# Kernel tuning notes

Measured on AMD Instinct MI355X. Metric: run time of the kernel, lower is better.

## Reference

```python
import jax, jax.numpy as jnp
import numpy as np

EPS = 1e-6

def _feature_map(x):
    # elu(x) + 1  (positive feature map)
    return jax.nn.elu(x) + 1.0

def setup_inputs() -> dict:
    key = jax.random.key(0)
    kq, kk, kv = jax.random.split(key, 3)
    N, L, S, H, D = 8, 4096, 4096, 8, 64
    return {
        "queries": jax.random.normal(kq, (N, L, H, D), dtype=jnp.float32),
        "keys": jax.random.normal(kk, (N, S, H, D), dtype=jnp.float32),
        "values": jax.random.normal(kv, (N, S, H, D), dtype=jnp.float32),
        "q_mask": jnp.ones((N, L), dtype=jnp.float32),
        "kv_mask": jnp.ones((N, S), dtype=jnp.float32),
    }

def reference(queries, keys, values, q_mask, kv_mask):
    Q = _feature_map(queries)                      # [N,L,H,D]
    K = _feature_map(keys)                         # [N,S,H,D]
    Q = Q * q_mask[:, :, None, None]
    kvm = kv_mask[:, :, None, None]
    K = K * kvm
    V = values * kvm
    S_len = V.shape[1]
    scale = 1.0 / S_len
    Vs = V * scale
    KV = jnp.einsum('nshd,nshv->nhdv', K, Vs)      # [N,H,D,D]
    # normalizer: Q . sum_s K   (intended math of the source einsum)
    Z = 1.0 / (jnp.einsum('nlhd,nhd->nlh', Q, K.sum(axis=1)) + EPS)
    out = jnp.einsum('nlhd,nhdv,nlh->nlhv', Q, KV, Z) * S_len
    return out
```

## Files before the change

kernel.cpp:

```cpp
#include <hip/hip_runtime.h>
#include <hip/hip_bf16.h>

#define NB 8
#define LQ 4096
#define SK 4096
#define NH 8
#define DD 64
#define NPAIR (NB*NH)
#define KVSZ (DD*DD + DD)
#define FRAGW 768

typedef short v8s __attribute__((ext_vector_type(8)));
typedef float v4f __attribute__((ext_vector_type(4)));
union U8 { v8s s; unsigned int u[4]; uint4 q; };

__device__ __forceinline__ float fmap(float x) {
    return x > 0.f ? x + 1.f : __expf(x);
}
__device__ __forceinline__ unsigned short bf_hi(float x) {
    unsigned int u = __float_as_uint(x);
    return (unsigned short)((u + 0x7FFFu + ((u >> 16) & 1u)) >> 16);
}
__device__ __forceinline__ float bf_f(unsigned short b) {
    return __uint_as_float(((unsigned int)b) << 16);
}
__device__ __forceinline__ uint2 packsplit2(float x0, float x1) {
    union { __hip_bfloat162 b; unsigned int u; } h, l;
    h.b = __float22bfloat162_rn(make_float2(x0, x1));
    float r0 = x0 - __uint_as_float(h.u << 16);
    float r1 = x1 - __uint_as_float(h.u & 0xFFFF0000u);
    l.b = __float22bfloat162_rn(make_float2(r0, r1));
    uint2 r; r.x = h.u; r.y = l.u;
    return r;
}
#define MFMA(A, B, C) __builtin_amdgcn_mfma_f32_16x16x32_bf16((A), (B), (C), 0, 0, 0)

__device__ __forceinline__ void gload16(const float* g, float* lds) {
    __builtin_amdgcn_global_load_lds(
        (const __attribute__((address_space(1))) unsigned int*)g,
        (__attribute__((address_space(3))) unsigned int*)lds, 16, 0, 0);
}

__global__ __launch_bounds__(256, 3) void kv_partial_kernel(
    const float* __restrict__ K, const float* __restrict__ V,
    const float* __restrict__ kvm, float* __restrict__ partial, int CH)
{
    int bx = blockIdx.x;
    int chunk = bx % CH;
    int pair  = bx / CH;
    int nb = pair >> 3, h = pair & 7;
    int tid = threadIdx.x, w = tid >> 6, lane = tid & 63;
    int g = lane >> 4, c16 = lane & 15;

    __shared__ float Kl[2][2048];
    __shared__ float Vl[2][2048];

    v4f acc[4];
    v4f z4 = {0.f, 0.f, 0.f, 0.f};
#pragma unroll
    for (int nn = 0; nn < 4; ++nn) acc[nn] = z4;
    float ksum = 0.f;

    int SC = SK / CH;
    int tiles = SC >> 5;
    int rowbase = nb * SK + chunk * SC;

    int srow0 = (lane >> 4);
    int dp    = (lane & 15) << 2;

    auto STAGE = [&](int b, int t) {
#pragma unroll
        for (int i = 0; i < 2; ++i) {
            int I = 2 * w + i;
            int s = I * 4 + srow0;
            int dl = dp ^ (((s >> 3) & 1) << 4);
            size_t gb = (size_t)(rowbase + (t << 5) + s) * (NH * DD) + h * DD + dl;
            gload16(K + gb, &Kl[b][I * 256]);
            gload16(V + gb, &Vl[b][I * 256]);
        }
    };

    auto COMPUTE = [&](int b, const float* mr) {
        float xa[8];
#pragma unroll
        for (int j = 0; j < 8; ++j) {
            int s = 8 * g + j;
            float kv_ = Kl[b][s * 64 + ((16 * w + c16) ^ (((s >> 3) & 1) << 4))];
            xa[j] = fmap(kv_) * mr[j];
            ksum += xa[j];
        }
        U8 ah, al;
#pragma unroll
        for (int p = 0; p < 4; ++p) {
            uint2 pw = packsplit2(xa[2 * p], xa[2 * p + 1]);
            ah.u[p] = pw.x; al.u[p] = pw.y;
        }
#pragma unroll
        for (int nn = 0; nn < 4; ++nn) {
            float xb[8];
#pragma unroll
            for (int j = 0; j < 8; ++j) {
                int s = 8 * g + j;
                xb[j] = Vl[b][s * 64 + ((16 * nn + c16) ^ (((s >> 3) & 1) << 4))] * mr[j];
            }
            U8 bh, bl;
#pragma unroll
            for (int p = 0; p < 4; ++p) {
                uint2 pw = packsplit2(xb[2 * p], xb[2 * p + 1]);
                bh.u[p] = pw.x; bl.u[p] = pw.y;
            }
            acc[nn] = MFMA(ah.s, bh.s, acc[nn]);
            acc[nn] = MFMA(al.s, bh.s, acc[nn]);
            acc[nn] = MFMA(ah.s, bl.s, acc[nn]);
        }
    };

    float mr0[8], mr1[8];
    auto MLOADR = [&](float* mr, int t) {
#pragma unroll
        for (int j = 0; j < 8; ++j)
            mr[j] = kvm[rowbase + (t << 5) + 8 * g + j];
    };

    STAGE(0, 0); MLOADR(mr0, 0);
    __syncthreads();
    for (int t = 0; t < tiles; t += 2) {
        if (t + 1 < tiles) { STAGE(1, t + 1); MLOADR(mr1, t + 1); }
        COMPUTE(0, mr0);
        __syncthreads();
        if (t + 1 < tiles) {
            if (t + 2 < tiles) { STAGE(0, t + 2); MLOADR(mr0, t + 2); }
            COMPUTE(1, mr1);
            __syncthreads();
        }
    }

    ksum += __shfl_xor(ksum, 16);
    ksum += __shfl_xor(ksum, 32);
    float* dst = partial + ((size_t)chunk * NPAIR + pair) * KVSZ;
    if (lane < 16) dst[4096 + 16 * w + c16] = ksum;
#pragma unroll
    for (int nn = 0; nn < 4; ++nn)
#pragma unroll
        for (int jj = 0; jj < 4; ++jj)
            dst[(16 * w + 4 * g + jj) * 64 + 16 * nn + c16] = acc[nn][jj];
}

__global__ __launch_bounds__(256) void kv_reduce_kernel(
    const float* __restrict__ partial, float* __restrict__ kvf, int CH)
{
    int i = blockIdx.x * 256 + threadIdx.x;
    if (i >= NPAIR * KVSZ) return;
    float s = 0.f;
    for (int c = 0; c < CH; ++c) s += partial[(size_t)c * NPAIR * KVSZ + i];
    kvf[i] = s;
}

__global__ __launch_bounds__(256) void kv_pack_kernel(
    const float* __restrict__ kvf, uint4* __restrict__ frag)
{
    int pair = blockIdx.x;
    int t = threadIdx.x;
    __shared__ float kvr[KVSZ];
    const float* src = kvf + (size_t)pair * KVSZ;
    for (int e = t; e < KVSZ / 4; e += 256)
        *(float4*)&kvr[4 * e] = *(const float4*)(src + 4 * e);
    __syncthreads();

    for (int e = t; e < FRAGW; e += 256) {
        int i4 = e >> 6, lane = e & 63;
        int g = lane >> 4, c16 = lane & 15;
        unsigned int wd[4];
        if (i4 < 8) {
            int ks = i4 >> 2, nn = i4 & 3;
#pragma unroll
            for (int p = 0; p < 4; ++p) {
                float x0 = kvr[(32 * ks + 8 * g + 2 * p) * 64 + 16 * nn + c16];
                float x1 = kvr[(32 * ks + 8 * g + 2 * p + 1) * 64 + 16 * nn + c16];
                wd[p] = (unsigned int)bf_hi(x0) | ((unsigned int)bf_hi(x1) << 16);
            }
        } else {
            int j = i4 - 8, ks = j & 1, lo = j >> 1;
#pragma unroll
            for (int p = 0; p < 4; ++p) {
                unsigned int wp = 0;
                if (c16 == 0) {
                    float x0 = kvr[4096 + 32 * ks + 8 * g + 2 * p];
                    float x1 = kvr[4096 + 32 * ks + 8 * g + 2 * p + 1];
                    unsigned short h0 = bf_hi(x0), h1 = bf_hi(x1);
                    if (lo)
                        wp = (unsigned int)bf_hi(x0 - bf_f(h0)) |
                             ((unsigned int)bf_hi(x1 - bf_f(h1)) << 16);
                    else
                        wp = (unsigned int)h0 | ((unsigned int)h1 << 16);
                }
                wd[p] = wp;
            }
        }
        uint4 o; o.x = wd[0]; o.y = wd[1]; o.z = wd[2]; o.w = wd[3];
        frag[(size_t)pair * FRAGW + e] = o;
    }
}

__global__ __launch_bounds__(256) void attn_out_kernel(
    const float* __restrict__ Q, const float* __restrict__ qm,
    const uint4* __restrict__ frag, float* __restrict__ out)
{
    int bx = blockIdx.x;
    int pair = bx >> 5;
    int rb   = bx & 31;
    int nb = pair >> 3, h = pair & 7;
    int lane = threadIdx.x & 63;
    int w    = threadIdx.x >> 6;
    int g    = lane >> 4;
    int c16  = lane & 15;

    const uint4* fb = frag + (size_t)pair * FRAGW;
    U8 Bh[2][4], Bkh[2], Bkl[2];
#pragma unroll
    for (int ks = 0; ks < 2; ++ks)
#pragma unroll
        for (int nn = 0; nn < 4; ++nn)
            Bh[ks][nn].q = fb[(ks * 4 + nn) * 64 + lane];
    Bkh[0].q = fb[8 * 64 + lane];
    Bkh[1].q = fb[9 * 64 + lane];
    Bkl[0].q = fb[10 * 64 + lane];
    Bkl[1].q = fb[11 * 64 + lane];

    float4 qA[2][4];
    float qmA[2];

    auto QLOAD = [&](int it, float4* qr, float& qmv) {
        int row = rb * 128 + (w + 4 * it) * 16 + c16;
        qmv = qm[nb * LQ + row];
        const float* qrow = Q + ((size_t)((nb * LQ + row) * NH + h)) * DD;
        qr[0] = *(const float4*)(qrow + 8 * g);
        qr[1] = *(const float4*)(qrow + 8 * g + 4);
        qr[2] = *(const float4*)(qrow + 8 * g + 32);
        qr[3] = *(const float4*)(qrow + 8 * g + 36);
    };

    v4f z4 = {0.f, 0.f, 0.f, 0.f};
    QLOAD(0, qA[0], qmA[0]);
#pragma unroll
    for (int it = 0; it < 2; ++it) {
        if (it == 0) QLOAD(1, qA[1], qmA[1]);
        const float4* qr = qA[it];
        float qmv = qmA[it];

        U8 Ah[2], Al[2];
#pragma unroll
        for (int ks = 0; ks < 2; ++ks) {
            float qv[8] = {qr[2*ks].x, qr[2*ks].y, qr[2*ks].z, qr[2*ks].w,
                           qr[2*ks+1].x, qr[2*ks+1].y, qr[2*ks+1].z, qr[2*ks+1].w};
#pragma unroll
            for (int p = 0; p < 4; ++p) {
                uint2 pw = packsplit2(fmap(qv[2*p]) * qmv, fmap(qv[2*p+1]) * qmv);
                Ah[ks].u[p] = pw.x;
                Al[ks].u[p] = pw.y;
            }
        }

        v4f a0 = z4, a1 = z4, a2 = z4, a3 = z4, a4 = z4;
#pragma unroll
        for (int ks = 0; ks < 2; ++ks) {
            a0 = MFMA(Ah[ks].s, Bh[ks][0].s, a0);
            a1 = MFMA(Ah[ks].s, Bh[ks][1].s, a1);
            a2 = MFMA(Ah[ks].s, Bh[ks][2].s, a2);
            a3 = MFMA(Ah[ks].s, Bh[ks][3].s, a3);
            a0 = MFMA(Al[ks].s, Bh[ks][0].s, a0);
            a1 = MFMA(Al[ks].s, Bh[ks][1].s, a1);
            a2 = MFMA(Al[ks].s, Bh[ks][2].s, a2);
            a3 = MFMA(Al[ks].s, Bh[ks][3].s, a3);
            a4 = MFMA(Ah[ks].s, Bkh[ks].s, a4);
            a4 = MFMA(Al[ks].s, Bkh[ks].s, a4);
            a4 = MFMA(Ah[ks].s, Bkl[ks].s, a4);
        }

        int row0 = rb * 128 + (w + 4 * it) * 16;
        int src = lane & 48;
#pragma unroll
        for (int jj = 0; jj < 4; ++jj) {
            float den = __shfl(a4[jj], src);
            float z = 1.f / (den + 1e-6f);
            size_t ob = ((size_t)((nb * LQ + row0 + 4 * g + jj) * NH + h)) * DD + c16;
            out[ob]      = a0[jj] * z;
            out[ob + 16] = a1[jj] * z;
            out[ob + 32] = a2[jj] * z;
            out[ob + 48] = a3[jj] * z;
        }
    }
}

extern "C" void kernel_launch(void* const* d_in, const int* in_sizes, int n_in,
                              void* d_out, int out_size, void* d_ws, size_t ws_size,
                              hipStream_t stream) {
    const float* Q   = (const float*)d_in[0];
    const float* K   = (const float*)d_in[1];
    const float* V   = (const float*)d_in[2];
    const float* qm  = (const float*)d_in[3];
    const float* kvm = (const float*)d_in[4];
    float* out = (float*)d_out;

    int CH = 16;
    while (CH > 1 && (size_t)(CH + 1) * NPAIR * KVSZ * sizeof(float) > ws_size) CH >>= 1;

    float* partial = (float*)d_ws;
    float* kvf = partial + (size_t)CH * NPAIR * KVSZ;
    uint4* frag = (uint4*)d_ws;

    kv_partial_kernel<<<dim3(NPAIR * CH), dim3(256), 0, stream>>>(K, V, kvm, partial, CH);
    kv_reduce_kernel<<<dim3((NPAIR * KVSZ + 255) / 256), dim3(256), 0, stream>>>(partial, kvf, CH);
    kv_pack_kernel<<<dim3(NPAIR), dim3(256), 0, stream>>>(kvf, frag);
    attn_out_kernel<<<dim3(NPAIR * 32), dim3(256), 0, stream>>>(Q, qm, frag, out);
}
```

Measured before the change: 81.93 us.

## Restructure KV partial kernel to load full rows across all heads per block

The KV-partial kernel now gives each 512-thread block one batch and sequence chunk across all 8 heads, one wave per head. It stages contiguous 2KB K/V rows (all heads) into LDS instead of strided 256B per-head slices. Each wave computes a full 64x64 KV tile with 16-row tiles, so half the lanes feed zeros into the MFMAs because the K=32 instruction is only half used. Chunk count doubles to 32, which doubles the partial-sum traffic through the reduce kernel, and register use per thread rises with 16 accumulators.

After: 93.35 us. +13.9%, slower.

```diff
diff --git a/kernel.cpp b/kernel.cpp
--- a/kernel.cpp
+++ b/kernel.cpp
@@ -9,6 +9,7 @@
 #define NPAIR (NB*NH)
 #define KVSZ (DD*DD + DD)
 #define FRAGW 768
+#define TS 16
 
 typedef short v8s __attribute__((ext_vector_type(8)));
 typedef float v4f __attribute__((ext_vector_type(4)));
@@ -41,109 +42,131 @@
         (__attribute__((address_space(3))) unsigned int*)lds, 16, 0, 0);
 }
 
-__global__ __launch_bounds__(256, 3) void kv_partial_kernel(
+__global__ __launch_bounds__(512, 2) void kv_partial_kernel(
     const float* __restrict__ K, const float* __restrict__ V,
     const float* __restrict__ kvm, float* __restrict__ partial, int CH)
 {
     int bx = blockIdx.x;
     int chunk = bx % CH;
-    int pair  = bx / CH;
-    int nb = pair >> 3, h = pair & 7;
+    int nb    = bx / CH;
     int tid = threadIdx.x, w = tid >> 6, lane = tid & 63;
     int g = lane >> 4, c16 = lane & 15;
 
-    __shared__ float Kl[2][2048];
-    __shared__ float Vl[2][2048];
-
-    v4f acc[4];
+    __shared__ float Kt[2][TS][512];
+    __shared__ float Vt[2][TS][512];
+
+    v4f acc[4][4];
     v4f z4 = {0.f, 0.f, 0.f, 0.f};
 #pragma unroll
-    for (int nn = 0; nn < 4; ++nn) acc[nn] = z4;
-    float ksum = 0.f;
+    for (int md = 0; md < 4; ++md)
+#pragma unroll
+        for (int nn = 0; nn < 4; ++nn) acc[md][nn] = z4;
+    float ksum[4] = {0.f, 0.f, 0.f, 0.f};
 
     int SC = SK / CH;
-    int tiles = SC >> 5;
+    int tiles = SC / TS;
     int rowbase = nb * SK + chunk * SC;
 
-    int srow0 = (lane >> 4);
-    int dp    = (lane & 15) << 2;
-
     auto STAGE = [&](int b, int t) {
 #pragma unroll
-        for (int i = 0; i < 2; ++i) {
-            int I = 2 * w + i;
-            int s = I * 4 + srow0;
-            int dl = dp ^ (((s >> 3) & 1) << 4);
-            size_t gb = (size_t)(rowbase + (t << 5) + s) * (NH * DD) + h * DD + dl;
-            gload16(K + gb, &Kl[b][I * 256]);
-            gload16(V + gb, &Vl[b][I * 256]);
+        for (int u = 0; u < 8; ++u) {
+            int unit = w * 8 + u;
+            int arr  = unit >> 5;
+            int row  = (unit >> 1) & 15;
+            int half = unit & 1;
+            size_t gb = ((size_t)(rowbase + t * TS + row)) * 512 + half * 256 + lane * 4;
+            if (arr == 0) gload16(K + gb, &Kt[b][row][half * 256]);
+            else          gload16(V + gb, &Vt[b][row][half * 256]);
         }
     };
 
+    auto MLOAD = [&](float* mr, int t) {
+        if (g < 2) {
+#pragma unroll
+            for (int j = 0; j < 8; ++j)
+                mr[j] = kvm[rowbase + t * TS + 8 * g + j];
+        }
+    };
+
     auto COMPUTE = [&](int b, const float* mr) {
-        float xa[8];
-#pragma unroll
-        for (int j = 0; j < 8; ++j) {
-            int s = 8 * g + j;
-            float kv_ = Kl[b][s * 64 + ((16 * w + c16) ^ (((s >> 3) & 1) << 4))];
-            xa[j] = fmap(kv_) * mr[j];
-            ksum += xa[j];
-        }
-        U8 ah, al;
-#pragma unroll
-        for (int p = 0; p < 4; ++p) {
-            uint2 pw = packsplit2(xa[2 * p], xa[2 * p + 1]);
-            ah.u[p] = pw.x; al.u[p] = pw.y;
-        }
+        U8 bh[4], bl[4];
 #pragma unroll
         for (int nn = 0; nn < 4; ++nn) {
-            float xb[8];
-#pragma unroll
-            for (int j = 0; j < 8; ++j) {
-                int s = 8 * g + j;
-                xb[j] = Vl[b][s * 64 + ((16 * nn + c16) ^ (((s >> 3) & 1) << 4))] * mr[j];
-            }
-            U8 bh, bl;
-#pragma unroll
-            for (int p = 0; p < 4; ++p) {
-                uint2 pw = packsplit2(xb[2 * p], xb[2 * p + 1]);
-                bh.u[p] = pw.x; bl.u[p] = pw.y;
-            }
-            acc[nn] = MFMA(ah.s, bh.s, acc[nn]);
-            acc[nn] = MFMA(al.s, bh.s, acc[nn]);
-            acc[nn] = MFMA(ah.s, bl.s, acc[nn]);
+            if (g < 2) {
+                float xb[8];
+#pragma unroll
+                for (int j = 0; j < 8; ++j)
+                    xb[j] = Vt[b][8 * g + j][w * 64 + 16 * nn + c16] * mr[j];
+#pragma unroll
+                for (int p = 0; p < 4; ++p) {
+                    uint2 pw = packsplit2(xb[2 * p], xb[2 * p + 1]);
+                    bh[nn].u[p] = pw.x; bl[nn].u[p] = pw.y;
+                }
+            } else {
+#pragma unroll
+                for (int p = 0; p < 4; ++p) { bh[nn].u[p] = 0u; bl[nn].u[p] = 0u; }
+            }
+        }
+#pragma unroll
+        for (int md = 0; md < 4; ++md) {
+            U8 ah, al;
+            if (g < 2) {
+                float xa[8];
+#pragma unroll
+                for (int j = 0; j < 8; ++j) {
+                    float x = fmap(Kt[b][8 * g + j][w * 64 + 16 * md + c16]) * mr[j];
+                    xa[j] = x;
+                    ksum[md] += x;
+                }
+#pragma unroll
+                for (int p = 0; p < 4; ++p) {
+                    uint2 pw = packsplit2(xa[2 * p], xa[2 * p + 1]);
+                    ah.u[p] = pw.x; al.u[p] = pw.y;
+                }
+            } else {
+#pragma unroll
+                for (int p = 0; p < 4; ++p) { ah.u[p] = 0u; al.u[p] = 0u; }
+            }
+#pragma unroll
+            for (int nn = 0; nn < 4; ++nn) {
+                acc[md][nn] = MFMA(ah.s, bh[nn].s, acc[md][nn]);
+                acc[md][nn] = MFMA(al.s, bh[nn].s, acc[md][nn]);
+                acc[md][nn] = MFMA(ah.s, bl[nn].s, acc[md][nn]);
+            }
         }
     };
 
-    float mr0[8], mr1[8];
-    auto MLOADR = [&](float* mr, int t) {
-#pragma unroll
-        for (int j = 0; j < 8; ++j)
-            mr[j] = kvm[rowbase + (t << 5) + 8 * g + j];
-    };
-
-    STAGE(0, 0); MLOADR(mr0, 0);
+    float mrA[8], mrB[8];
+    STAGE(0, 0); MLOAD(mrA, 0);
     __syncthreads();
     for (int t = 0; t < tiles; t += 2) {
-        if (t + 1 < tiles) { STAGE(1, t + 1); MLOADR(mr1, t + 1); }
-        COMPUTE(0, mr0);
+        if (t + 1 < tiles) { STAGE(1, t + 1); MLOAD(mrB, t + 1); }
+        COMPUTE(0, mrA);
         __syncthreads();
         if (t + 1 < tiles) {
-            if (t + 2 < tiles) { STAGE(0, t + 2); MLOADR(mr0, t + 2); }
-            COMPUTE(1, mr1);
+            if (t + 2 < tiles) { STAGE(0, t + 2); MLOAD(mrA, t + 2); }
+            COMPUTE(1, mrB);
             __syncthreads();
         }
     }
 
-    ksum += __shfl_xor(ksum, 16);
-    ksum += __shfl_xor(ksum, 32);
+#pragma unroll
+    for (int md = 0; md < 4; ++md) {
+        ksum[md] += __shfl_xor(ksum[md], 16);
+        ksum[md] += __shfl_xor(ksum[md], 32);
+    }
+    int pair = nb * 8 + w;
     float* dst = partial + ((size_t)chunk * NPAIR + pair) * KVSZ;
-    if (lane < 16) dst[4096 + 16 * w + c16] = ksum;
-#pragma unroll
-    for (int nn = 0; nn < 4; ++nn)
-#pragma unroll
-        for (int jj = 0; jj < 4; ++jj)
-            dst[(16 * w + 4 * g + jj) * 64 + 16 * nn + c16] = acc[nn][jj];
+    if (lane < 16)
+#pragma unroll
+        for (int md = 0; md < 4; ++md) dst[4096 + 16 * md + c16] = ksum[md];
+#pragma unroll
+    for (int md = 0; md < 4; ++md)
+#pragma unroll
+        for (int nn = 0; nn < 4; ++nn)
+#pragma unroll
+            for (int jj = 0; jj < 4; ++jj)
+                dst[(16 * md + 4 * g + jj) * 64 + 16 * nn + c16] = acc[md][nn][jj];
 }
 
 __global__ __launch_bounds__(256) void kv_reduce_kernel(
@@ -302,14 +325,14 @@
     const float* kvm = (const float*)d_in[4];
     float* out = (float*)d_out;
 
-    int CH = 16;
+    int CH = 32;
     while (CH > 1 && (size_t)(CH + 1) * NPAIR * KVSZ * sizeof(float) > ws_size) CH >>= 1;
 
     float* partial = (float*)d_ws;
     float* kvf = partial + (size_t)CH * NPAIR * KVSZ;
     uint4* frag = (uint4*)d_ws;
 
-    kv_partial_kernel<<<dim3(NPAIR * CH), dim3(256), 0, stream>>>(K, V, kvm, partial, CH);
+    kv_partial_kernel<<<dim3(NB * CH), dim3(512), 0, stream>>>(K, V, kvm, partial, CH);
     kv_reduce_kernel<<<dim3((NPAIR * KVSZ + 255) / 256), dim3(256), 0, stream>>>(partial, kvf, CH);
     kv_pack_kernel<<<dim3(NPAIR), dim3(256), 0, stream>>>(kvf, frag);
     attn_out_kernel<<<dim3(NPAIR * 32), dim3(256), 0, stream>>>(Q, qm, frag, out);
```

## Load K/V directly to registers with 2x2 MFMA tiles per wave

Applied to the files above, without the earlier changes.

Rewrites the KV partial kernel to drop the double-buffered LDS staging and barriers, with each thread loading its K and V elements straight from global memory into registers. Each wave now computes a 2x2 block of 16x16 tiles, a 32-row slice of the D dimension by a 32-column slice of V, instead of a 16x64 strip, so each wave converts fewer V fragments per step. The chunk count rises to 32 and the occupancy hint to 4 blocks per CU to expose more parallelism. The cost is strided, less coalesced 4-byte global loads with no prefetch overlap, and a larger partial buffer for the reduce kernel to read.

Measured after the change: 88.29 us. 1.08x slower.

```diff
diff --git a/kernel.cpp b/kernel.cpp
--- a/kernel.cpp
+++ b/kernel.cpp
@@ -35,13 +35,7 @@
 }
 #define MFMA(A, B, C) __builtin_amdgcn_mfma_f32_16x16x32_bf16((A), (B), (C), 0, 0, 0)
 
-__device__ __forceinline__ void gload16(const float* g, float* lds) {
-    __builtin_amdgcn_global_load_lds(
-        (const __attribute__((address_space(1))) unsigned int*)g,
-        (__attribute__((address_space(3))) unsigned int*)lds, 16, 0, 0);
-}
-
-__global__ __launch_bounds__(256, 3) void kv_partial_kernel(
+__global__ __launch_bounds__(256, 4) void kv_partial_kernel(
     const float* __restrict__ K, const float* __restrict__ V,
     const float* __restrict__ kvm, float* __restrict__ partial, int CH)
 {
@@ -51,99 +45,88 @@
     int nb = pair >> 3, h = pair & 7;
     int tid = threadIdx.x, w = tid >> 6, lane = tid & 63;
     int g = lane >> 4, c16 = lane & 15;
-
-    __shared__ float Kl[2][2048];
-    __shared__ float Vl[2][2048];
-
-    v4f acc[4];
+    int dh = w >> 1, vh = w & 1;
+
+    v4f acc[2][2];
     v4f z4 = {0.f, 0.f, 0.f, 0.f};
-#pragma unroll
-    for (int nn = 0; nn < 4; ++nn) acc[nn] = z4;
-    float ksum = 0.f;
+    acc[0][0] = z4; acc[0][1] = z4; acc[1][0] = z4; acc[1][1] = z4;
+    float ksum[2] = {0.f, 0.f};
 
     int SC = SK / CH;
     int tiles = SC >> 5;
     int rowbase = nb * SK + chunk * SC;
 
-    int srow0 = (lane >> 4);
-    int dp    = (lane & 15) << 2;
-
-    auto STAGE = [&](int b, int t) {
-#pragma unroll
-        for (int i = 0; i < 2; ++i) {
-            int I = 2 * w + i;
-            int s = I * 4 + srow0;
-            int dl = dp ^ (((s >> 3) & 1) << 4);
-            size_t gb = (size_t)(rowbase + (t << 5) + s) * (NH * DD) + h * DD + dl;
-            gload16(K + gb, &Kl[b][I * 256]);
-            gload16(V + gb, &Vl[b][I * 256]);
-        }
-    };
-
-    auto COMPUTE = [&](int b, const float* mr) {
-        float xa[8];
+    const float* Kp = K + (size_t)rowbase * (NH * DD) + h * DD + 32 * dh + c16;
+    const float* Vp = V + (size_t)rowbase * (NH * DD) + h * DD + 32 * vh + c16;
+    const float* Mp = kvm + rowbase + 8 * g;
+
+    for (int t = 0; t < tiles; ++t) {
+        float kb[16], vb[16], mb[8];
+        int s0 = (t << 5) + 8 * g;
 #pragma unroll
         for (int j = 0; j < 8; ++j) {
-            int s = 8 * g + j;
-            float kv_ = Kl[b][s * 64 + ((16 * w + c16) ^ (((s >> 3) & 1) << 4))];
-            xa[j] = fmap(kv_) * mr[j];
-            ksum += xa[j];
-        }
-        U8 ah, al;
-#pragma unroll
-        for (int p = 0; p < 4; ++p) {
-            uint2 pw = packsplit2(xa[2 * p], xa[2 * p + 1]);
-            ah.u[p] = pw.x; al.u[p] = pw.y;
-        }
-#pragma unroll
-        for (int nn = 0; nn < 4; ++nn) {
+            size_t off = (size_t)(s0 + j) * (NH * DD);
+            mb[j]     = Mp[(t << 5) + j];
+            kb[j]     = Kp[off];
+            kb[8 + j] = Kp[off + 16];
+            vb[j]     = Vp[off];
+            vb[8 + j] = Vp[off + 16];
+        }
+        U8 ah[2], al[2], bh[2], bl[2];
+#pragma unroll
+        for (int m = 0; m < 2; ++m) {
+            float xa[8];
+#pragma unroll
+            for (int j = 0; j < 8; ++j) xa[j] = fmap(kb[m * 8 + j]) * mb[j];
+            if (vh == 0) {
+#pragma unroll
+                for (int j = 0; j < 8; ++j) ksum[m] += xa[j];
+            }
+#pragma unroll
+            for (int p = 0; p < 4; ++p) {
+                uint2 pw = packsplit2(xa[2 * p], xa[2 * p + 1]);
+                ah[m].u[p] = pw.x; al[m].u[p] = pw.y;
+            }
+        }
+#pragma unroll
+        for (int n = 0; n < 2; ++n) {
             float xb[8];
 #pragma unroll
-            for (int j = 0; j < 8; ++j) {
-                int s = 8 * g + j;
-                xb[j] = Vl[b][s * 64 + ((16 * nn + c16) ^ (((s >> 3) & 1) << 4))] * mr[j];
-            }
-            U8 bh, bl;
+            for (int j = 0; j < 8; ++j) xb[j] = vb[n * 8 + j] * mb[j];
 #pragma unroll
             for (int p = 0; p < 4; ++p) {
                 uint2 pw = packsplit2(xb[2 * p], xb[2 * p + 1]);
-                bh.u[p] = pw.x; bl.u[p] = pw.y;
-            }
-            acc[nn] = MFMA(ah.s, bh.s, acc[nn]);
-            acc[nn] = MFMA(al.s, bh.s, acc[nn]);
-            acc[nn] = MFMA(ah.s, bl.s, acc[nn]);
-        }
-    };
-
-    float mr0[8], mr1[8];
-    auto MLOADR = [&](float* mr, int t) {
-#pragma unroll
-        for (int j = 0; j < 8; ++j)
-            mr[j] = kvm[rowbase + (t << 5) + 8 * g + j];
-    };
-
-    STAGE(0, 0); MLOADR(mr0, 0);
-    __syncthreads();
-    for (int t = 0; t < tiles; t += 2) {
-        if (t + 1 < tiles) { STAGE(1, t + 1); MLOADR(mr1, t + 1); }
-        COMPUTE(0, mr0);
-        __syncthreads();
-        if (t + 1 < tiles) {
-            if (t + 2 < tiles) { STAGE(0, t + 2); MLOADR(mr0, t + 2); }
-            COMPUTE(1, mr1);
-            __syncthreads();
-        }
-    }
-
-    ksum += __shfl_xor(ksum, 16);
-    ksum += __shfl_xor(ksum, 32);
+                bh[n].u[p] = pw.x; bl[n].u[p] = pw.y;
+            }
+        }
+#pragma unroll
+        for (int m = 0; m < 2; ++m)
+#pragma unroll
+            for (int n = 0; n < 2; ++n) {
+                acc[m][n] = MFMA(ah[m].s, bh[n].s, acc[m][n]);
+                acc[m][n] = MFMA(al[m].s, bh[n].s, acc[m][n]);
+                acc[m][n] = MFMA(ah[m].s, bl[n].s, acc[m][n]);
+            }
+    }
+
+#pragma unroll
+    for (int m = 0; m < 2; ++m) {
+        ksum[m] += __shfl_xor(ksum[m], 16);
+        ksum[m] += __shfl_xor(ksum[m], 32);
+    }
     float* dst = partial + ((size_t)chunk * NPAIR + pair) * KVSZ;
-    if (lane < 16) dst[4096 + 16 * w + c16] = ksum;
-#pragma unroll
-    for (int nn = 0; nn < 4; ++nn)
-#pragma unroll
-        for (int jj = 0; jj < 4; ++jj)
-            dst[(16 * w + 4 * g + jj) * 64 + 16 * nn + c16] = acc[nn][jj];
+    if (vh == 0 && lane < 16) {
+        dst[4096 + 32 * dh + c16]      = ksum[0];
+        dst[4096 + 32 * dh + 16 + c16] = ksum[1];
+    }
+#pragma unroll
+    for (int m = 0; m < 2; ++m)
+#pragma unroll
+        for (int n = 0; n < 2; ++n)
+#pragma unroll
+            for (int jj = 0; jj < 4; ++jj)
+                dst[(32 * dh + 16 * m + 4 * g + jj) * 64 + 32 * vh + 16 * n + c16]
+                    = acc[m][n][jj];
 }
 
 __global__ __launch_bounds__(256) void kv_reduce_kernel(
@@ -302,7 +285,7 @@
     const float* kvm = (const float*)d_in[4];
     float* out = (float*)d_out;
 
-    int CH = 16;
+    int CH = 32;
     while (CH > 1 && (size_t)(CH + 1) * NPAIR * KVSZ * sizeof(float) > ws_size) CH >>= 1;
 
     float* partial = (float*)d_ws;
```
